# Performance work log

Hardware: AMD Instinct MI355X
Metric: run time of the kernel (lower is better)

Reference implementation:

```python
import jax, jax.numpy as jnp
import numpy as np

H = 8
DK = 32  # head_dim = 256 // 8
SCALE = 1.0 / np.float32(np.sqrt(DK))
EPS = 1e-5


def _ln(x, g, b):
    mu = jnp.mean(x, axis=-1, keepdims=True)
    var = jnp.var(x, axis=-1, keepdims=True)
    return (x - mu) / jnp.sqrt(var + EPS) * g + b


def _lin(x, W, b):
    return x @ W + b


def setup_inputs() -> dict:
    key = jax.random.key(0)
    ks = jax.random.split(key, 16)
    B, M, N, D, F = 4, 64, 512, 256, 1024
    s = 0.02
    inp = {
        "machine_emb": jax.random.normal(ks[0], (B, M, D), jnp.float32),
        "op_emb": jax.random.normal(ks[1], (B, N, D), jnp.float32),
        "edge_emb": jax.random.normal(ks[2], (B, N, M, D), jnp.float32),
        "o2m_mask": jax.random.bernoulli(ks[3], 0.3, (B, N, M)),
    }
    # projection weights stored as (in, out)
    for i, nm in enumerate(["q", "k", "v", "o", "ks", "vs", "e"]):
        inp["W" + nm] = jax.random.normal(ks[4 + i], (D, D), jnp.float32) * s
        inp["b" + nm] = jnp.zeros((D,), jnp.float32)
    # layernorms: norm1 (g1/b1), norm2 (g2/b2), norm_op (gop/bop)
    for nm in ["1", "2", "op"]:
        inp["g" + nm] = jnp.ones((D,), jnp.float32)
        inp["bn" + nm] = jnp.zeros((D,), jnp.float32)
    # FFN
    inp["Wf1"] = jax.random.normal(ks[11], (D, F), jnp.float32) * s
    inp["bf1"] = jnp.zeros((F,), jnp.float32)
    inp["Wf2"] = jax.random.normal(ks[12], (F, D), jnp.float32) * s
    inp["bf2"] = jnp.zeros((D,), jnp.float32)
    return inp


def reference(machine_emb, op_emb, edge_emb, o2m_mask,
              Wq, bq, Wk, bk, Wv, bv, Wo, bo, Wks, bks, Wvs, bvs, We, be,
              g1, bn1, g2, bn2, gop, bnop, Wf1, bf1, Wf2, bf2):
    B, M, D = machine_emb.shape
    N = op_emb.shape[1]

    residual = machine_emb
    machine_norm = _ln(machine_emb, g1, bn1)
    op_norm = _ln(op_emb, gop, bnop)

    # (B, H, M, dk) / (B, H, N, dk)
    q_m = _lin(machine_norm, Wq, bq).reshape(B, M, H, DK).transpose(0, 2, 1, 3)
    k_o = _lin(op_norm, Wk, bk).reshape(B, N, H, DK).transpose(0, 2, 1, 3)
    v_o = _lin(op_norm, Wv, bv).reshape(B, N, H, DK).transpose(0, 2, 1, 3)

    # edge: (B,N,M,D) -> (B,H,M,N,dk)
    edge = _lin(edge_emb, We, be).reshape(B, N, M, H, DK)
    edge = edge.transpose(0, 3, 2, 1, 4)  # bhmnd

    q_total = q_m[:, :, :, None, :] + edge          # (B,H,M,N,dk)
    k_total = k_o[:, :, None, :, :] + edge          # (B,H,M,N,dk)
    v_total = v_o[:, :, None, :, :] + edge          # (B,H,M,N,dk)

    scores = jnp.sum(q_total * k_total, axis=-1) * SCALE  # (B,H,M,N)

    k_self = _lin(machine_norm, Wks, bks).reshape(B, M, H, DK).transpose(0, 2, 1, 3)
    self_scores = jnp.sum(q_m * k_self, axis=-1) * SCALE   # (B,H,M)

    cross_mask = o2m_mask.transpose(0, 2, 1)[:, None, :, :]  # (B,1,M,N)
    combined_scores = jnp.concatenate([self_scores[..., None], scores], axis=-1)  # (B,H,M,1+N)
    self_flag = jnp.ones((B, 1, M, 1), dtype=bool)
    combined_mask = jnp.concatenate([self_flag, jnp.broadcast_to(cross_mask, (B, 1, M, N))], axis=-1)
    combined_scores = jnp.where(combined_mask, combined_scores, -jnp.inf)

    attn = jax.nn.softmax(combined_scores, axis=-1)
    attn = jnp.where(jnp.isnan(attn), 0.0, attn)

    v_self = _lin(machine_norm, Wvs, bvs).reshape(B, M, H, DK).transpose(0, 2, 1, 3)
    combined_values = jnp.concatenate([v_self[:, :, :, None, :], v_total], axis=3)  # (B,H,M,1+N,dk)

    attn_out = jnp.einsum('bhmi,bhmid->bhmd', attn, combined_values)
    attn_out = attn_out.transpose(0, 2, 1, 3).reshape(B, M, D)
    attn_out = _lin(attn_out, Wo, bo)

    machine_emb = residual + attn_out
    h = _ln(machine_emb, g2, bn2)
    ffn = _lin(jax.nn.relu(_lin(h, Wf1, bf1)), Wf2, bf2)
    return machine_emb + ffn
```

## Files before the change

kernel.cpp:

```cpp
#include <hip/hip_runtime.h>
#include <hip/hip_bf16.h>
#include <math.h>

#define H_ 8
#define DK_ 32
#define B_ 4
#define M_ 64
#define N_ 512
#define D_ 256
#define F_ 1024

static constexpr float SCALE = 0.17677669529663687f;
static constexpr float EPS = 1e-5f;

typedef __bf16 bf16x8 __attribute__((ext_vector_type(8)));
typedef float f32x4 __attribute__((ext_vector_type(4)));

__device__ inline float bfbits2f(unsigned int b) {
    union { unsigned int i; float f; } c; c.i = b << 16; return c.f;
}
__device__ inline void unpack8(uint4 u, float* f) {
    f[0] = bfbits2f(u.x & 0xffffu); f[1] = bfbits2f(u.x >> 16);
    f[2] = bfbits2f(u.y & 0xffffu); f[3] = bfbits2f(u.y >> 16);
    f[4] = bfbits2f(u.z & 0xffffu); f[5] = bfbits2f(u.z >> 16);
    f[6] = bfbits2f(u.w & 0xffffu); f[7] = bfbits2f(u.w >> 16);
}

__global__ __launch_bounds__(256) void detect_kernel(const unsigned int* __restrict__ mask,
                                                     int* __restrict__ flags) {
    __shared__ int s2[256];
    int t = threadIdx.x;
    int cgt = 0;
    for (int i = 0; i < 128; ++i) {
        unsigned int w = mask[t * 128 + i];
        if (w > 1u) cgt++;
    }
    s2[t] = cgt;
    __syncthreads();
    if (t == 0) {
        int b = 0;
        for (int i = 0; i < 256; ++i) b += s2[i];
        flags[1] = (b > 0) ? 1 : 0;
    }
}

__global__ __launch_bounds__(256) void conv_maskT_kernel(const void* __restrict__ src,
                                                         const int* __restrict__ flags,
                                                         int* __restrict__ dst) {
    int i = blockIdx.x * 256 + threadIdx.x;
    int b = i >> 15, m = (i >> 9) & 63, n = i & 511;
    int si = (b * 512 + n) * 64 + m;
    bool u8 = flags[1] != 0;
    dst[i] = u8 ? (int)((const unsigned char*)src)[si] : ((const int*)src)[si];
}

struct TransArgs {
    const void* src[9];
    void* dst[9];
    int cum[9];
    int kl[9];
    int nl[9];
};

__global__ __launch_bounds__(256) void prep_transpose(TransArgs a, int total) {
    int i = blockIdx.x * 256 + threadIdx.x;
    if (i >= total) return;
    int t = 0;
    while (i >= a.cum[t]) t++;
    int j = i - (t == 0 ? 0 : a.cum[t - 1]);
    int K = 1 << a.kl[t];
    int n = j >> a.kl[t];
    int k = j & (K - 1);
    float v = ((const float*)a.src[t])[((size_t)k << a.nl[t]) + n];
    ((__hip_bfloat16*)a.dst[t])[j] = __float2bfloat16(v);
}

__global__ __launch_bounds__(256) void prep_bias(const float* bq, const float* bks,
                                                 const float* bvs, const float* bk,
                                                 const float* bv,
                                                 float* bqksvs, float* bkv) {
    int t = threadIdx.x;
    bqksvs[t] = bq[t];
    bqksvs[256 + t] = bks[t];
    bqksvs[512 + t] = bvs[t];
    bkv[t] = bk[t];
    bkv[256 + t] = bv[t];
}

__device__ inline float block_reduce256(float v, bool is_max, float* sbuf) {
#pragma unroll
    for (int off = 32; off > 0; off >>= 1) {
        float o = __shfl_down(v, off, 64);
        v = is_max ? fmaxf(v, o) : (v + o);
    }
    int lane = threadIdx.x & 63, wid = threadIdx.x >> 6;
    if (lane == 0) sbuf[wid] = v;
    __syncthreads();
    float r;
    if (is_max) r = fmaxf(fmaxf(sbuf[0], sbuf[1]), fmaxf(sbuf[2], sbuf[3]));
    else        r = sbuf[0] + sbuf[1] + sbuf[2] + sbuf[3];
    __syncthreads();
    return r;
}

__global__ __launch_bounds__(256) void ln_kernel(const float* __restrict__ xin,
                                                 const float* __restrict__ g,
                                                 const float* __restrict__ bta,
                                                 __hip_bfloat16* __restrict__ out) {
    __shared__ float sbuf[4];
    int row = blockIdx.x, d = threadIdx.x;
    size_t idx = (size_t)row * 256 + d;
    float x = xin[idx];
    float s  = block_reduce256(x, false, sbuf);
    float ss = block_reduce256(x * x, false, sbuf);
    float mu = s * (1.f / 256.f);
    float var = ss * (1.f / 256.f) - mu * mu;
    float y = (x - mu) * rsqrtf(var + EPS) * g[d] + bta[d];
    out[idx] = __float2bfloat16(y);
}

__global__ __launch_bounds__(256) void gemm64(const __hip_bfloat16* __restrict__ A,
                                              const __hip_bfloat16* __restrict__ BT,
                                              const float* __restrict__ bias,
                                              const float* __restrict__ resid,
                                              void* __restrict__ out,
                                              int K, int ldc, int flags) {
    __shared__ __align__(16) __bf16 As[64 * 32];
    __shared__ __align__(16) __bf16 Bs[64 * 32];
    const int rowBase = blockIdx.x * 64;
    const int colBase = blockIdx.y * 64;
    const int t = threadIdx.x;
    const int w = t >> 6;
    const int l = t & 63;
    const int lrow = l & 15;
    const int lk8 = (l >> 4) * 8;
    const int ar = t >> 2;
    const int ac = (t & 3) * 8;

    f32x4 acc[4] = {};
    for (int k0 = 0; k0 < K; k0 += 32) {
        bf16x8 av = *(const bf16x8*)(A + (size_t)(rowBase + ar) * K + k0 + ac);
        bf16x8 bv = *(const bf16x8*)(BT + (size_t)(colBase + ar) * K + k0 + ac);
        __syncthreads();
        *(bf16x8*)(As + ar * 32 + ac) = av;
        *(bf16x8*)(Bs + ar * 32 + ac) = bv;
        __syncthreads();
        bf16x8 af = *(const bf16x8*)(As + (w * 16 + lrow) * 32 + lk8);
#pragma unroll
        for (int c = 0; c < 4; ++c) {
            bf16x8 bf = *(const bf16x8*)(Bs + (c * 16 + lrow) * 32 + lk8);
            acc[c] = __builtin_amdgcn_mfma_f32_16x16x32_bf16(af, bf, acc[c], 0, 0, 0);
        }
    }
    int rbase = rowBase + w * 16 + ((l >> 4) * 4);
#pragma unroll
    for (int c = 0; c < 4; ++c) {
        int col = colBase + c * 16 + (l & 15);
        float bb = bias[col];
#pragma unroll
        for (int r = 0; r < 4; ++r) {
            int row = rbase + r;
            size_t oi = (size_t)row * ldc + col;
            float v = acc[c][r] + bb;
            if (flags & 1) v = fmaxf(v, 0.f);
            if (flags & 4) v += resid[oi];
            if (flags & 8) ((float*)out)[oi] = v;
            else ((__hip_bfloat16*)out)[oi] = __float2bfloat16(v);
        }
    }
}

__global__ __launch_bounds__(256) void edge_gemm2(const float* __restrict__ E,
                                                  const __hip_bfloat16* __restrict__ WeT,
                                                  const float* __restrict__ be,
                                                  __hip_bfloat16* __restrict__ eperm) {
    __shared__ __align__(16) char smem[64 * 272 * 2];
    __bf16* As = (__bf16*)smem;
    __bf16* Bs = (__bf16*)(smem + 4096);
    __bf16* Cs = (__bf16*)smem;
    const int bn = blockIdx.x;
    const int t = threadIdx.x;
    const int w = t >> 6;
    const int l = t & 63;
    const int lrow = l & 15;
    const int lk8 = (l >> 4) * 8;
    const int ar = t >> 2;
    const int ac = (t & 3) * 8;
    const float* Ab = E + (size_t)bn * 64 * 256;

    f32x4 acc[4][4] = {};
    for (int k0 = 0; k0 < 256; k0 += 32) {
        const float* ap = Ab + (size_t)ar * 256 + k0 + ac;
        float4 x0 = *(const float4*)ap;
        float4 x1 = *(const float4*)(ap + 4);
        bf16x8 av;
        av[0] = (__bf16)x0.x; av[1] = (__bf16)x0.y; av[2] = (__bf16)x0.z; av[3] = (__bf16)x0.w;
        av[4] = (__bf16)x1.x; av[5] = (__bf16)x1.y; av[6] = (__bf16)x1.z; av[7] = (__bf16)x1.w;
        bf16x8 bv[4];
#pragma unroll
        for (int j = 0; j < 4; ++j)
            bv[j] = *(const bf16x8*)(WeT + (size_t)t * 256 + k0 + j * 8);
        __syncthreads();
        *(bf16x8*)(As + ar * 32 + ac) = av;
#pragma unroll
        for (int j = 0; j < 4; ++j)
            *(bf16x8*)(Bs + t * 32 + j * 8) = bv[j];
        __syncthreads();
        bf16x8 af[4];
#pragma unroll
        for (int rr = 0; rr < 4; ++rr)
            af[rr] = *(const bf16x8*)(As + (rr * 16 + lrow) * 32 + lk8);
#pragma unroll
        for (int c = 0; c < 4; ++c) {
            bf16x8 bf = *(const bf16x8*)(Bs + (w * 64 + c * 16 + lrow) * 32 + lk8);
#pragma unroll
            for (int rr = 0; rr < 4; ++rr)
                acc[rr][c] = __builtin_amdgcn_mfma_f32_16x16x32_bf16(af[rr], bf, acc[rr][c], 0, 0, 0);
        }
    }
    __syncthreads();
#pragma unroll
    for (int c = 0; c < 4; ++c) {
        int col = w * 64 + c * 16 + (l & 15);
        float bb = be[col];
#pragma unroll
        for (int rr = 0; rr < 4; ++rr) {
#pragma unroll
            for (int r = 0; r < 4; ++r) {
                int m = rr * 16 + (l >> 4) * 4 + r;
                Cs[m * 272 + col] = (__bf16)(acc[rr][c][r] + bb);
            }
        }
    }
    __syncthreads();
    int b = bn >> 9, n = bn & 511;
#pragma unroll
    for (int j = 0; j < 8; ++j) {
        int flat = j * 256 + t;
        int m = flat >> 5, seg = flat & 31;
        int h = seg >> 2, dk8 = (seg & 3) * 8;
        size_t oi = (((size_t)((b * 8 + h) * 64 + m) * 512) + n) * 32 + dk8;
        *(uint4*)(eperm + oi) = *(const uint4*)(Cs + m * 272 + seg * 8);
    }
}

__global__ __launch_bounds__(256) void scores_kernel(const __hip_bfloat16* __restrict__ qkvs,
                                                     const __hip_bfloat16* __restrict__ kov,
                                                     const __hip_bfloat16* __restrict__ eperm,
                                                     const int* __restrict__ maskT,
                                                     float* __restrict__ S) {
    int bhm = blockIdx.x;
    int m = bhm & 63;
    int h = (bhm >> 6) & 7;
    int b = bhm >> 9;
    __shared__ float sq[32];
    int t = threadIdx.x;
    int w = t >> 6, l = t & 63;
    if (t < 32) sq[t] = __bfloat162float(qkvs[(size_t)(b * 64 + m) * 768 + h * 32 + t]);
    __syncthreads();
    float qv[32];
#pragma unroll
    for (int i = 0; i < 32; ++i) qv[i] = sq[i];
    const __hip_bfloat16* ebase = eperm + (size_t)bhm * 512 * 32;

    for (int it = 0; it < 2; ++it) {
        int n = w * 128 + it * 64 + l;
        float kv[32], ev[32];
        const uint4* kp = (const uint4*)(kov + (size_t)(b * 512 + n) * 512 + h * 32);
        const uint4* ep = (const uint4*)(ebase + (size_t)n * 32);
#pragma unroll
        for (int i = 0; i < 4; ++i) unpack8(kp[i], kv + 8 * i);
#pragma unroll
        for (int i = 0; i < 4; ++i) unpack8(ep[i], ev + 8 * i);
        float s = 0.f;
#pragma unroll
        for (int i = 0; i < 32; ++i) {
            float e = ev[i];
            s += (qv[i] + e) * (kv[i] + e);
        }
        int mk = maskT[(size_t)(b * 64 + m) * 512 + n];
        S[(size_t)bhm * 512 + n] = mk ? s * SCALE : -__builtin_inff();
    }
}

__global__ __launch_bounds__(256) void softmax_kernel(const float* __restrict__ S,
                                                      const __hip_bfloat16* __restrict__ qkvs,
                                                      float* __restrict__ attn,
                                                      float* __restrict__ attn_self) {
    __shared__ float sbuf[4];
    __shared__ float sself;
    int bhm = blockIdx.x;
    int m = bhm & 63;
    int h = (bhm >> 6) & 7;
    int b = bhm >> 9;
    int t = threadIdx.x;
    if (t == 0) {
        const __hip_bfloat16* q  = qkvs + (size_t)(b * 64 + m) * 768 + h * 32;
        const __hip_bfloat16* ks = qkvs + (size_t)(b * 64 + m) * 768 + 256 + h * 32;
        float s = 0.f;
        for (int i = 0; i < 32; ++i) s += __bfloat162float(q[i]) * __bfloat162float(ks[i]);
        sself = s * SCALE;
    }
    __syncthreads();
    float sv = sself;
    float s0 = S[(size_t)bhm * 512 + t];
    float s1 = S[(size_t)bhm * 512 + 256 + t];
    float mx = fmaxf(fmaxf(s0, s1), sv);
    mx = block_reduce256(mx, true, sbuf);
    float e0 = __expf(s0 - mx);
    float e1 = __expf(s1 - mx);
    float eself = __expf(sv - mx);
    float part = e0 + e1 + (t == 0 ? eself : 0.f);
    float sum = block_reduce256(part, false, sbuf);
    float inv = 1.f / sum;
    attn[(size_t)bhm * 512 + t] = e0 * inv;
    attn[(size_t)bhm * 512 + 256 + t] = e1 * inv;
    if (t == 0) attn_self[bhm] = eself * inv;
}

__global__ __launch_bounds__(256) void attnout_kernel(const float* __restrict__ attn,
                                                      const float* __restrict__ attn_self,
                                                      const __hip_bfloat16* __restrict__ kov,
                                                      const __hip_bfloat16* __restrict__ qkvs,
                                                      const __hip_bfloat16* __restrict__ eperm,
                                                      __hip_bfloat16* __restrict__ AO) {
    int bhm = blockIdx.x;
    int m = bhm & 63;
    int h = (bhm >> 6) & 7;
    int b = bhm >> 9;
    int t = threadIdx.x;
    int s = t >> 5, d = t & 31;
    const __hip_bfloat16* ebase = eperm + (size_t)bhm * 512 * 32;
    float acc = 0.f;
    for (int n = s; n < 512; n += 8) {
        float a = attn[(size_t)bhm * 512 + n];
        float e = __bfloat162float(ebase[(size_t)n * 32 + d]);
        float v = __bfloat162float(kov[(size_t)(b * 512 + n) * 512 + 256 + h * 32 + d]);
        acc += a * (v + e);
    }
    __shared__ float red[256];
    red[t] = acc;
    __syncthreads();
    if (s == 0) {
        float r = red[d] + red[32 + d] + red[64 + d] + red[96 + d]
                + red[128 + d] + red[160 + d] + red[192 + d] + red[224 + d];
        float vs = __bfloat162float(qkvs[(size_t)(b * 64 + m) * 768 + 512 + h * 32 + d]);
        r += attn_self[bhm] * vs;
        AO[(size_t)(b * 64 + m) * 256 + h * 32 + d] = __float2bfloat16(r);
    }
}

extern "C" void kernel_launch(void* const* d_in, const int* in_sizes, int n_in,
                              void* d_out, int out_size, void* d_ws, size_t ws_size,
                              hipStream_t stream) {
    const float* machine_emb = (const float*)d_in[0];
    const float* op_emb      = (const float*)d_in[1];
    const float* edge_emb    = (const float*)d_in[2];
    const void*  o2m_mask    = d_in[3];

    char* p = (char*)d_ws;
    int* flags = (int*)p;                        p += 256;
    int* maskT = (int*)p;                        p += 131072 * 4;
    __hip_bfloat16* WqksvsT = (__hip_bfloat16*)p; p += 196608 * 2;
    __hip_bfloat16* WkvT    = (__hip_bfloat16*)p; p += 131072 * 2;
    __hip_bfloat16* WoT     = (__hip_bfloat16*)p; p += 65536 * 2;
    __hip_bfloat16* WeT     = (__hip_bfloat16*)p; p += 65536 * 2;
    __hip_bfloat16* Wf1T    = (__hip_bfloat16*)p; p += 262144 * 2;
    __hip_bfloat16* Wf2T    = (__hip_bfloat16*)p; p += 262144 * 2;
    float* bqksvs           = (float*)p;          p += 768 * 4;
    float* bkv              = (float*)p;          p += 512 * 4;
    __hip_bfloat16* mnorm   = (__hip_bfloat16*)p; p += 65536 * 2;
    __hip_bfloat16* onorm   = (__hip_bfloat16*)p; p += 524288 * 2;
    __hip_bfloat16* qkvs    = (__hip_bfloat16*)p; p += 196608 * 2;
    __hip_bfloat16* kov     = (__hip_bfloat16*)p; p += 1048576 * 2;
    __hip_bfloat16* eperm   = (__hip_bfloat16*)p; p += (size_t)33554432 * 2;
    float* sc        = (float*)p;                p += (size_t)1048576 * 4;
    float* attn      = (float*)p;                p += (size_t)1048576 * 4;
    float* attn_self = (float*)p;                p += 2048 * 4;
    __hip_bfloat16* AO = (__hip_bfloat16*)p;     p += 65536 * 2;
    float* m2        = (float*)p;                p += 65536 * 4;
    __hip_bfloat16* hn = (__hip_bfloat16*)p;     p += 65536 * 2;
    __hip_bfloat16* h1 = (__hip_bfloat16*)p;     p += 262144 * 2;

    TransArgs ta;
    const int srcIdx[9] = {4, 12, 14, 6, 8, 10, 16, 24, 26};
    void* dsts[9] = {WqksvsT, WqksvsT + 65536, WqksvsT + 131072,
                     WkvT, WkvT + 65536, WoT, WeT, Wf1T, Wf2T};
    const int sizes9[9] = {65536, 65536, 65536, 65536, 65536, 65536, 65536, 262144, 262144};
    const int kl9[9] = {8, 8, 8, 8, 8, 8, 8, 8, 10};
    const int nl9[9] = {8, 8, 8, 8, 8, 8, 8, 10, 8};
    int cum = 0;
    for (int i = 0; i < 9; ++i) {
        ta.src[i] = d_in[srcIdx[i]];
        ta.dst[i] = dsts[i];
        cum += sizes9[i];
        ta.cum[i] = cum;
        ta.kl[i] = kl9[i];
        ta.nl[i] = nl9[i];
    }

    hipLaunchKernelGGL(detect_kernel, dim3(1), dim3(256), 0, stream,
                       (const unsigned int*)o2m_mask, flags);
    hipLaunchKernelGGL(prep_transpose, dim3((cum + 255) / 256), dim3(256), 0, stream, ta, cum);
    hipLaunchKernelGGL(prep_bias, dim3(1), dim3(256), 0, stream,
                       (const float*)d_in[5], (const float*)d_in[13],
                       (const float*)d_in[15], (const float*)d_in[7],
                       (const float*)d_in[9], bqksvs, bkv);
    hipLaunchKernelGGL(conv_maskT_kernel, dim3(512), dim3(256), 0, stream, o2m_mask, flags, maskT);

    hipLaunchKernelGGL(ln_kernel, dim3(256), dim3(256), 0, stream,
                       machine_emb, (const float*)d_in[18], (const float*)d_in[19], mnorm);
    hipLaunchKernelGGL(ln_kernel, dim3(2048), dim3(256), 0, stream,
                       op_emb, (const float*)d_in[22], (const float*)d_in[23], onorm);

    hipLaunchKernelGGL(gemm64, dim3(4, 12), dim3(256), 0, stream,
                       mnorm, WqksvsT, bqksvs, nullptr, qkvs, 256, 768, 0);
    hipLaunchKernelGGL(gemm64, dim3(32, 8), dim3(256), 0, stream,
                       onorm, WkvT, bkv, nullptr, kov, 256, 512, 0);

    hipLaunchKernelGGL(edge_gemm2, dim3(2048), dim3(256), 0, stream,
                       edge_emb, WeT, (const float*)d_in[17], eperm);

    hipLaunchKernelGGL(scores_kernel, dim3(2048), dim3(256), 0, stream, qkvs, kov, eperm, maskT, sc);
    hipLaunchKernelGGL(softmax_kernel, dim3(2048), dim3(256), 0, stream, sc, qkvs, attn, attn_self);
    hipLaunchKernelGGL(attnout_kernel, dim3(2048), dim3(256), 0, stream,
                       attn, attn_self, kov, qkvs, eperm, AO);

    hipLaunchKernelGGL(gemm64, dim3(4, 4), dim3(256), 0, stream,
                       AO, WoT, (const float*)d_in[11], machine_emb, m2, 256, 256, 4 | 8);
    hipLaunchKernelGGL(ln_kernel, dim3(256), dim3(256), 0, stream,
                       m2, (const float*)d_in[20], (const float*)d_in[21], hn);
    hipLaunchKernelGGL(gemm64, dim3(4, 16), dim3(256), 0, stream,
                       hn, Wf1T, (const float*)d_in[25], nullptr, h1, 256, 1024, 1);
    hipLaunchKernelGGL(gemm64, dim3(4, 4), dim3(256), 0, stream,
                       h1, Wf2T, (const float*)d_in[27], m2, (float*)d_out, 1024, 256, 4 | 8);
}
```

Baseline: 403.8 us.

## Fuse score computation into edge GEMM and merge softmax with attention output

```diff
diff --git a/kernel.cpp b/kernel.cpp
--- a/kernel.cpp
+++ b/kernel.cpp
@@ -42,16 +42,6 @@
         for (int i = 0; i < 256; ++i) b += s2[i];
         flags[1] = (b > 0) ? 1 : 0;
     }
-}
-
-__global__ __launch_bounds__(256) void conv_maskT_kernel(const void* __restrict__ src,
-                                                         const int* __restrict__ flags,
-                                                         int* __restrict__ dst) {
-    int i = blockIdx.x * 256 + threadIdx.x;
-    int b = i >> 15, m = (i >> 9) & 63, n = i & 511;
-    int si = (b * 512 + n) * 64 + m;
-    bool u8 = flags[1] != 0;
-    dst[i] = u8 ? (int)((const unsigned char*)src)[si] : ((const int*)src)[si];
 }
 
 struct TransArgs {
@@ -170,55 +160,46 @@
     }
 }
 
-__global__ __launch_bounds__(256) void edge_gemm2(const float* __restrict__ E,
+__global__ __launch_bounds__(256) void edge_gemm3(const float* __restrict__ E,
                                                   const __hip_bfloat16* __restrict__ WeT,
                                                   const float* __restrict__ be,
-                                                  __hip_bfloat16* __restrict__ eperm) {
-    __shared__ __align__(16) char smem[64 * 272 * 2];
-    __bf16* As = (__bf16*)smem;
-    __bf16* Bs = (__bf16*)(smem + 4096);
-    __bf16* Cs = (__bf16*)smem;
+                                                  const __hip_bfloat16* __restrict__ qkvs,
+                                                  const __hip_bfloat16* __restrict__ kov,
+                                                  const void* __restrict__ mask,
+                                                  const int* __restrict__ flags,
+                                                  __hip_bfloat16* __restrict__ eperm,
+                                                  float* __restrict__ sc) {
+    __shared__ __align__(16) __bf16 Cs[64 * 272];
     const int bn = blockIdx.x;
+    const int b = bn >> 9, n = bn & 511;
     const int t = threadIdx.x;
     const int w = t >> 6;
     const int l = t & 63;
     const int lrow = l & 15;
     const int lk8 = (l >> 4) * 8;
-    const int ar = t >> 2;
-    const int ac = (t & 3) * 8;
     const float* Ab = E + (size_t)bn * 64 * 256;
 
     f32x4 acc[4][4] = {};
     for (int k0 = 0; k0 < 256; k0 += 32) {
-        const float* ap = Ab + (size_t)ar * 256 + k0 + ac;
-        float4 x0 = *(const float4*)ap;
-        float4 x1 = *(const float4*)(ap + 4);
-        bf16x8 av;
-        av[0] = (__bf16)x0.x; av[1] = (__bf16)x0.y; av[2] = (__bf16)x0.z; av[3] = (__bf16)x0.w;
-        av[4] = (__bf16)x1.x; av[5] = (__bf16)x1.y; av[6] = (__bf16)x1.z; av[7] = (__bf16)x1.w;
-        bf16x8 bv[4];
-#pragma unroll
-        for (int j = 0; j < 4; ++j)
-            bv[j] = *(const bf16x8*)(WeT + (size_t)t * 256 + k0 + j * 8);
-        __syncthreads();
-        *(bf16x8*)(As + ar * 32 + ac) = av;
-#pragma unroll
-        for (int j = 0; j < 4; ++j)
-            *(bf16x8*)(Bs + t * 32 + j * 8) = bv[j];
-        __syncthreads();
         bf16x8 af[4];
 #pragma unroll
-        for (int rr = 0; rr < 4; ++rr)
-            af[rr] = *(const bf16x8*)(As + (rr * 16 + lrow) * 32 + lk8);
+        for (int rr = 0; rr < 4; ++rr) {
+            const float* ap = Ab + (size_t)(rr * 16 + lrow) * 256 + k0 + lk8;
+            float4 x0 = *(const float4*)ap;
+            float4 x1 = *(const float4*)(ap + 4);
+            af[rr][0] = (__bf16)x0.x; af[rr][1] = (__bf16)x0.y;
+            af[rr][2] = (__bf16)x0.z; af[rr][3] = (__bf16)x0.w;
+            af[rr][4] = (__bf16)x1.x; af[rr][5] = (__bf16)x1.y;
+            af[rr][6] = (__bf16)x1.z; af[rr][7] = (__bf16)x1.w;
+        }
 #pragma unroll
         for (int c = 0; c < 4; ++c) {
-            bf16x8 bf = *(const bf16x8*)(Bs + (w * 64 + c * 16 + lrow) * 32 + lk8);
+            bf16x8 bf = *(const bf16x8*)(WeT + (size_t)(w * 64 + c * 16 + lrow) * 256 + k0 + lk8);
 #pragma unroll
             for (int rr = 0; rr < 4; ++rr)
                 acc[rr][c] = __builtin_amdgcn_mfma_f32_16x16x32_bf16(af[rr], bf, acc[rr][c], 0, 0, 0);
         }
     }
-    __syncthreads();
 #pragma unroll
     for (int c = 0; c < 4; ++c) {
         int col = w * 64 + c * 16 + (l & 15);
@@ -233,62 +214,46 @@
         }
     }
     __syncthreads();
-    int b = bn >> 9, n = bn & 511;
+    const bool u8 = flags[1] != 0;
+    const int seg = t & 31;
+    const int h = seg >> 2;
+    const int dk8 = (seg & 3) * 8;
 #pragma unroll
     for (int j = 0; j < 8; ++j) {
-        int flat = j * 256 + t;
-        int m = flat >> 5, seg = flat & 31;
-        int h = seg >> 2, dk8 = (seg & 3) * 8;
-        size_t oi = (((size_t)((b * 8 + h) * 64 + m) * 512) + n) * 32 + dk8;
-        *(uint4*)(eperm + oi) = *(const uint4*)(Cs + m * 272 + seg * 8);
-    }
-}
-
-__global__ __launch_bounds__(256) void scores_kernel(const __hip_bfloat16* __restrict__ qkvs,
-                                                     const __hip_bfloat16* __restrict__ kov,
-                                                     const __hip_bfloat16* __restrict__ eperm,
-                                                     const int* __restrict__ maskT,
-                                                     float* __restrict__ S) {
-    int bhm = blockIdx.x;
-    int m = bhm & 63;
-    int h = (bhm >> 6) & 7;
-    int b = bhm >> 9;
-    __shared__ float sq[32];
-    int t = threadIdx.x;
-    int w = t >> 6, l = t & 63;
-    if (t < 32) sq[t] = __bfloat162float(qkvs[(size_t)(b * 64 + m) * 768 + h * 32 + t]);
-    __syncthreads();
-    float qv[32];
-#pragma unroll
-    for (int i = 0; i < 32; ++i) qv[i] = sq[i];
-    const __hip_bfloat16* ebase = eperm + (size_t)bhm * 512 * 32;
-
-    for (int it = 0; it < 2; ++it) {
-        int n = w * 128 + it * 64 + l;
-        float kv[32], ev[32];
-        const uint4* kp = (const uint4*)(kov + (size_t)(b * 512 + n) * 512 + h * 32);
-        const uint4* ep = (const uint4*)(ebase + (size_t)n * 32);
-#pragma unroll
-        for (int i = 0; i < 4; ++i) unpack8(kp[i], kv + 8 * i);
-#pragma unroll
-        for (int i = 0; i < 4; ++i) unpack8(ep[i], ev + 8 * i);
-        float s = 0.f;
-#pragma unroll
-        for (int i = 0; i < 32; ++i) {
-            float e = ev[i];
-            s += (qv[i] + e) * (kv[i] + e);
-        }
-        int mk = maskT[(size_t)(b * 64 + m) * 512 + n];
-        S[(size_t)bhm * 512 + n] = mk ? s * SCALE : -__builtin_inff();
-    }
-}
-
-__global__ __launch_bounds__(256) void softmax_kernel(const float* __restrict__ S,
-                                                      const __hip_bfloat16* __restrict__ qkvs,
-                                                      float* __restrict__ attn,
-                                                      float* __restrict__ attn_self) {
+        int m = j * 8 + (t >> 5);
+        uint4 ev4 = *(const uint4*)(Cs + m * 272 + seg * 8);
+        size_t bhm = (size_t)((b * 8 + h) * 64 + m);
+        *(uint4*)(eperm + (bhm * 512 + n) * 32 + dk8) = ev4;
+        float ev[8], qf[8], kf[8];
+        unpack8(ev4, ev);
+        uint4 qv4 = *(const uint4*)(qkvs + (size_t)(b * 64 + m) * 768 + h * 32 + dk8);
+        uint4 kv4 = *(const uint4*)(kov + (size_t)(b * 512 + n) * 512 + h * 32 + dk8);
+        unpack8(qv4, qf);
+        unpack8(kv4, kf);
+        float p = 0.f;
+#pragma unroll
+        for (int i = 0; i < 8; ++i)
+            p += (qf[i] + ev[i]) * (kf[i] + ev[i]);
+        p += __shfl_xor(p, 1, 64);
+        p += __shfl_xor(p, 2, 64);
+        if ((t & 3) == 0) {
+            int mi = (b * 512 + n) * 64 + m;
+            int mk = u8 ? (int)((const unsigned char*)mask)[mi] : ((const int*)mask)[mi];
+            sc[bhm * 512 + n] = mk ? p * SCALE : -__builtin_inff();
+        }
+    }
+}
+
+__global__ __launch_bounds__(256) void smax_attnout(const float* __restrict__ sc,
+                                                    const __hip_bfloat16* __restrict__ qkvs,
+                                                    const __hip_bfloat16* __restrict__ kov,
+                                                    const __hip_bfloat16* __restrict__ eperm,
+                                                    __hip_bfloat16* __restrict__ AO) {
     __shared__ float sbuf[4];
-    __shared__ float sself;
+    __shared__ float attnS[512];
+    __shared__ float selfSc;
+    __shared__ float selfA;
+    __shared__ float red[16][8];
     int bhm = blockIdx.x;
     int m = bhm & 63;
     int h = (bhm >> 6) & 7;
@@ -296,57 +261,60 @@
     int t = threadIdx.x;
     if (t == 0) {
         const __hip_bfloat16* q  = qkvs + (size_t)(b * 64 + m) * 768 + h * 32;
-        const __hip_bfloat16* ks = qkvs + (size_t)(b * 64 + m) * 768 + 256 + h * 32;
+        const __hip_bfloat16* ks = q + 256;
         float s = 0.f;
         for (int i = 0; i < 32; ++i) s += __bfloat162float(q[i]) * __bfloat162float(ks[i]);
-        sself = s * SCALE;
-    }
-    __syncthreads();
-    float sv = sself;
-    float s0 = S[(size_t)bhm * 512 + t];
-    float s1 = S[(size_t)bhm * 512 + 256 + t];
-    float mx = fmaxf(fmaxf(s0, s1), sv);
-    mx = block_reduce256(mx, true, sbuf);
+        selfSc = s * SCALE;
+    }
+    __syncthreads();
+    float sv = selfSc;
+    float s0 = sc[(size_t)bhm * 512 + t];
+    float s1 = sc[(size_t)bhm * 512 + 256 + t];
+    float mx = block_reduce256(fmaxf(fmaxf(s0, s1), sv), true, sbuf);
     float e0 = __expf(s0 - mx);
     float e1 = __expf(s1 - mx);
     float eself = __expf(sv - mx);
-    float part = e0 + e1 + (t == 0 ? eself : 0.f);
-    float sum = block_reduce256(part, false, sbuf);
+    float sum = block_reduce256(e0 + e1 + (t == 0 ? eself : 0.f), false, sbuf);
     float inv = 1.f / sum;
-    attn[(size_t)bhm * 512 + t] = e0 * inv;
-    attn[(size_t)bhm * 512 + 256 + t] = e1 * inv;
-    if (t == 0) attn_self[bhm] = eself * inv;
-}
-
-__global__ __launch_bounds__(256) void attnout_kernel(const float* __restrict__ attn,
-                                                      const float* __restrict__ attn_self,
-                                                      const __hip_bfloat16* __restrict__ kov,
-                                                      const __hip_bfloat16* __restrict__ qkvs,
-                                                      const __hip_bfloat16* __restrict__ eperm,
-                                                      __hip_bfloat16* __restrict__ AO) {
-    int bhm = blockIdx.x;
-    int m = bhm & 63;
-    int h = (bhm >> 6) & 7;
-    int b = bhm >> 9;
-    int t = threadIdx.x;
-    int s = t >> 5, d = t & 31;
+    attnS[t] = e0 * inv;
+    attnS[256 + t] = e1 * inv;
+    if (t == 0) selfA = eself * inv;
+    __syncthreads();
+
+    const int d8 = (t & 3) * 8;
+    const int ng = t >> 2;
+    const int w = t >> 6, l = t & 63;
     const __hip_bfloat16* ebase = eperm + (size_t)bhm * 512 * 32;
-    float acc = 0.f;
-    for (int n = s; n < 512; n += 8) {
-        float a = attn[(size_t)bhm * 512 + n];
-        float e = __bfloat162float(ebase[(size_t)n * 32 + d]);
-        float v = __bfloat162float(kov[(size_t)(b * 512 + n) * 512 + 256 + h * 32 + d]);
-        acc += a * (v + e);
-    }
-    __shared__ float red[256];
-    red[t] = acc;
-    __syncthreads();
-    if (s == 0) {
-        float r = red[d] + red[32 + d] + red[64 + d] + red[96 + d]
-                + red[128 + d] + red[160 + d] + red[192 + d] + red[224 + d];
-        float vs = __bfloat162float(qkvs[(size_t)(b * 64 + m) * 768 + 512 + h * 32 + d]);
-        r += attn_self[bhm] * vs;
-        AO[(size_t)(b * 64 + m) * 256 + h * 32 + d] = __float2bfloat16(r);
+    const __hip_bfloat16* vbase = kov + (size_t)(b * 512) * 512 + 256 + h * 32;
+    float accv[8] = {};
+#pragma unroll
+    for (int i = 0; i < 8; ++i) {
+        int n = ng + i * 64;
+        float a = attnS[n];
+        float ev[8], vv[8];
+        uint4 e4 = *(const uint4*)(ebase + (size_t)n * 32 + d8);
+        uint4 v4 = *(const uint4*)(vbase + (size_t)n * 512 + d8);
+        unpack8(e4, ev);
+        unpack8(v4, vv);
+#pragma unroll
+        for (int k = 0; k < 8; ++k) accv[k] += a * (vv[k] + ev[k]);
+    }
+#pragma unroll
+    for (int off = 4; off <= 32; off <<= 1) {
+#pragma unroll
+        for (int k = 0; k < 8; ++k) accv[k] += __shfl_xor(accv[k], off, 64);
+    }
+    if ((l >> 2) == 0) {
+#pragma unroll
+        for (int k = 0; k < 8; ++k) red[w * 4 + (l & 3)][k] = accv[k];
+    }
+    __syncthreads();
+    if (t < 32) {
+        int slot = t >> 3, elem = t & 7;
+        float r = red[slot][elem] + red[4 + slot][elem] + red[8 + slot][elem] + red[12 + slot][elem];
+        float vs = __bfloat162float(qkvs[(size_t)(b * 64 + m) * 768 + 512 + h * 32 + t]);
+        r += selfA * vs;
+        AO[(size_t)(b * 64 + m) * 256 + h * 32 + t] = __float2bfloat16(r);
     }
 }
 
@@ -360,7 +328,6 @@
 
     char* p = (char*)d_ws;
     int* flags = (int*)p;                        p += 256;
-    int* maskT = (int*)p;                        p += 131072 * 4;
     __hip_bfloat16* WqksvsT = (__hip_bfloat16*)p; p += 196608 * 2;
     __hip_bfloat16* WkvT    = (__hip_bfloat16*)p; p += 131072 * 2;
     __hip_bfloat16* WoT     = (__hip_bfloat16*)p; p += 65536 * 2;
@@ -375,8 +342,6 @@
     __hip_bfloat16* kov     = (__hip_bfloat16*)p; p += 1048576 * 2;
     __hip_bfloat16* eperm   = (__hip_bfloat16*)p; p += (size_t)33554432 * 2;
     float* sc        = (float*)p;                p += (size_t)1048576 * 4;
-    float* attn      = (float*)p;                p += (size_t)1048576 * 4;
-    float* attn_self = (float*)p;                p += 2048 * 4;
     __hip_bfloat16* AO = (__hip_bfloat16*)p;     p += 65536 * 2;
     float* m2        = (float*)p;                p += 65536 * 4;
     __hip_bfloat16* hn = (__hip_bfloat16*)p;     p += 65536 * 2;
@@ -406,7 +371,6 @@
                        (const float*)d_in[5], (const float*)d_in[13],
                        (const float*)d_in[15], (const float*)d_in[7],
                        (const float*)d_in[9], bqksvs, bkv);
-    hipLaunchKernelGGL(conv_maskT_kernel, dim3(512), dim3(256), 0, stream, o2m_mask, flags, maskT);
 
     hipLaunchKernelGGL(ln_kernel, dim3(256), dim3(256), 0, stream,
                        machine_emb, (const float*)d_in[18], (const float*)d_in[19], mnorm);
@@ -418,13 +382,12 @@
     hipLaunchKernelGGL(gemm64, dim3(32, 8), dim3(256), 0, stream,
                        onorm, WkvT, bkv, nullptr, kov, 256, 512, 0);
 
-    hipLaunchKernelGGL(edge_gemm2, dim3(2048), dim3(256), 0, stream,
-                       edge_emb, WeT, (const float*)d_in[17], eperm);
-
-    hipLaunchKernelGGL(scores_kernel, dim3(2048), dim3(256), 0, stream, qkvs, kov, eperm, maskT, sc);
-    hipLaunchKernelGGL(softmax_kernel, dim3(2048), dim3(256), 0, stream, sc, qkvs, attn, attn_self);
-    hipLaunchKernelGGL(attnout_kernel, dim3(2048), dim3(256), 0, stream,
-                       attn, attn_self, kov, qkvs, eperm, AO);
+    hipLaunchKernelGGL(edge_gemm3, dim3(2048), dim3(256), 0, stream,
+                       edge_emb, WeT, (const float*)d_in[17],
+                       qkvs, kov, o2m_mask, flags, eperm, sc);
+
+    hipLaunchKernelGGL(smax_attnout, dim3(2048), dim3(256), 0, stream,
+                       sc, qkvs, kov, eperm, AO);
 
     hipLaunchKernelGGL(gemm64, dim3(4, 4), dim3(256), 0, stream,
                        AO, WoT, (const float*)d_in[11], machine_emb, m2, 256, 256, 4 | 8);
```

Result: slower. 451.8 us (+11.9%).
